# Kernel tuning notes

Hardware: AMD Instinct MI355X
Metric: run time of the kernel (lower is better)

## Reference

```python
import jax, jax.numpy as jnp
import numpy as np

B, DIN, DOUT, DC, K, DB = 4096, 512, 512, 64, 16, 256
NEG = 0.01
LN_EPS = 1e-5

def _lrelu(v):
    return jnp.where(v >= 0, v, NEG * v)

def setup_inputs() -> dict:
    key = jax.random.key(0)
    ks = jax.random.split(key, 12)
    bound = 1.0 / np.sqrt(DIN)
    def u(k, shape, b):
        return jax.random.uniform(k, shape, jnp.float32, -b, b)
    return {
        "x": jax.random.normal(ks[0], (B, DIN), jnp.float32),
        "c": jax.random.normal(ks[1], (B, DC), jnp.float32),
        "ln_gamma": jnp.ones((DIN,), jnp.float32),
        "ln_beta": jnp.zeros((DIN,), jnp.float32),
        "w1": u(ks[2], (DC, DB), 1.0 / np.sqrt(DC)),
        "b1": u(ks[3], (DB,), 1.0 / np.sqrt(DC)),
        "wr": u(ks[4], (DB, DB), 1.0 / np.sqrt(DB)),
        "br": u(ks[5], (DB,), 1.0 / np.sqrt(DB)),
        "w2": u(ks[6], (DB, K), 1.0 / np.sqrt(DB)),
        "b2": u(ks[7], (K,), 1.0 / np.sqrt(DB)),
        "W": u(ks[8], (K, DIN, DOUT), bound),
        "bvec": u(ks[9], (K, DOUT), bound),
    }

def reference(x, c, ln_gamma, ln_beta, w1, b1, wr, br, w2, b2, W, bvec):
    # DenseActivation: LayerNorm + LeakyReLU (dropout_rate=0)
    mu = jnp.mean(x, axis=-1, keepdims=True)
    var = jnp.mean(jnp.square(x - mu), axis=-1, keepdims=True)
    xn = (x - mu) * jax.lax.rsqrt(var + LN_EPS) * ln_gamma + ln_beta
    a = _lrelu(xn)  # [B, DIN]
    # basis_functions(c): Linear -> 1 preactivation resnet block -> LeakyReLU -> Linear
    h = c @ w1 + b1                      # [B, DB]
    h = h + (_lrelu(h) @ wr + br)        # residual block (preactivation)
    h = _lrelu(h)                        # activate_output
    bf = h @ w2 + b2                     # [B, K]
    # out_b = x_b^T (sum_k bf_bk W_k) + bf_b @ bias ; reordered contraction
    xw = jnp.einsum("bi,kio->bko", a, W)       # [B, K, DOUT]
    out = jnp.einsum("bk,bko->bo", bf, xw)     # [B, DOUT]
    out = out + bf @ bvec
    return out
```

## Files before the change

### kernel.cpp

```cpp
#include <hip/hip_runtime.h>


#define LRELU(v) ((v) >= 0.f ? (v) : 0.01f * (v))

typedef _Float16 f16x8 __attribute__((ext_vector_type(8)));
typedef float f32x4 __attribute__((ext_vector_type(4)));

#define GL16(gp, lp) __builtin_amdgcn_global_load_lds(                      \
    (const __attribute__((address_space(1))) void*)(gp),                    \
    (__attribute__((address_space(3))) void*)(lp), 16, 0, 0)

#define MFMA16(a, b, c) __builtin_amdgcn_mfma_f32_16x16x32_f16((a), (b), (c), 0, 0, 0)

__global__ __launch_bounds__(256) void prep_kernel(
    const float* __restrict__ x, const float* __restrict__ gam,
    const float* __restrict__ bet, _Float16* __restrict__ a,
    const float* __restrict__ c, const float* __restrict__ w1,
    const float* __restrict__ b1, const float* __restrict__ wr,
    const float* __restrict__ br, const float* __restrict__ w2,
    const float* __restrict__ b2, float* __restrict__ bfo,
    const float* __restrict__ W, _Float16* __restrict__ Wt)
{
    __shared__ __align__(16) char smem[18432];
    int tid = threadIdx.x;
    int blk = blockIdx.x;

    if (blk < 512) {
        float* c_l  = (float*)smem;
        float* lr_l = (float*)(smem + 2048);
        float* h_l  = (float*)(smem + 10240);
        int b0 = blk * 8;

        for (int i = tid; i < 8 * 64; i += 256) c_l[i] = c[(size_t)b0 * 64 + i];

        float w1c[64];
#pragma unroll
        for (int u = 0; u < 64; ++u) w1c[u] = w1[u * 256 + tid];
        float b1s = b1[tid];
        __syncthreads();

        float h1[8];
#pragma unroll
        for (int r = 0; r < 8; ++r) h1[r] = b1s;
#pragma unroll
        for (int j4 = 0; j4 < 16; ++j4) {
#pragma unroll
            for (int r = 0; r < 8; ++r) {
                float4 cv = *(const float4*)&c_l[r * 64 + j4 * 4];
                h1[r] += cv.x * w1c[j4 * 4 + 0] + cv.y * w1c[j4 * 4 + 1] +
                         cv.z * w1c[j4 * 4 + 2] + cv.w * w1c[j4 * 4 + 3];
            }
        }
#pragma unroll
        for (int r = 0; r < 8; ++r) lr_l[r * 256 + tid] = LRELU(h1[r]);
        __syncthreads();

        float brv = br[tid];
        float h2[8];
#pragma unroll
        for (int r = 0; r < 8; ++r) h2[r] = h1[r] + brv;

#pragma unroll 1
        for (int jc = 0; jc < 8; ++jc) {
            float w8[32];
#pragma unroll
            for (int u = 0; u < 32; ++u) w8[u] = wr[(jc * 32 + u) * 256 + tid];
#pragma unroll
            for (int j4 = 0; j4 < 8; ++j4) {
#pragma unroll
                for (int r = 0; r < 8; ++r) {
                    float4 lv = *(const float4*)&lr_l[r * 256 + jc * 32 + j4 * 4];
                    h2[r] += lv.x * w8[j4 * 4 + 0] + lv.y * w8[j4 * 4 + 1] +
                             lv.z * w8[j4 * 4 + 2] + lv.w * w8[j4 * 4 + 3];
                }
            }
        }
#pragma unroll
        for (int r = 0; r < 8; ++r) h_l[r * 256 + tid] = LRELU(h2[r]);
        __syncthreads();

        if (tid < 128) {
            int r = tid >> 4, k = tid & 15;
            float s = b2[k];
#pragma unroll 1
            for (int qc = 0; qc < 8; ++qc) {
                float wv[32];
#pragma unroll
                for (int u = 0; u < 32; ++u) wv[u] = w2[(qc * 32 + u) * 16 + k];
#pragma unroll
                for (int q4 = 0; q4 < 8; ++q4) {
                    float4 hv = *(const float4*)&h_l[r * 256 + qc * 32 + q4 * 4];
                    s += hv.x * wv[q4 * 4 + 0] + hv.y * wv[q4 * 4 + 1] +
                         hv.z * wv[q4 * 4 + 2] + hv.w * wv[q4 * 4 + 3];
                }
            }
            bfo[(size_t)(b0 + r) * 16 + k] = s;
        }

    } else if (blk < 1536) {
        float* t = (float*)smem;
        int bid = blk - 512;
        int k  = bid >> 6;
        int it = (bid >> 3) & 7;
        int ot = bid & 7;
        int i0 = it * 64, o0 = ot * 64;

        int rr = tid >> 4, c4 = (tid & 15) * 4;
#pragma unroll
        for (int p = 0; p < 4; ++p) {
            int r = p * 16 + rr;
            float4 v = *(const float4*)&W[((size_t)(k * 512 + i0 + r)) * 512 + o0 + c4];
            t[r * 65 + c4 + 0] = v.x;
            t[r * 65 + c4 + 1] = v.y;
            t[r * 65 + c4 + 2] = v.z;
            t[r * 65 + c4 + 3] = v.w;
        }
        __syncthreads();

        int ol = tid >> 2, c0 = (tid & 3) * 16;
        _Float16 hb[16] __attribute__((aligned(16)));
#pragma unroll
        for (int u = 0; u < 16; ++u) hb[u] = (_Float16)t[(c0 + u) * 65 + ol];
        _Float16* dst = &Wt[(size_t)(o0 + ol) * 8192 + k * 512 + i0 + c0];
        *(float4*)dst       = *(const float4*)&hb[0];
        *(float4*)(dst + 8) = *(const float4*)&hb[8];

    } else {
        int lane = tid & 63;
        int row  = (blk - 1536) * 4 + (tid >> 6);
        const float* xr = x + (size_t)row * 512 + lane * 8;
        float4 v0 = *(const float4*)xr;
        float4 v1 = *(const float4*)(xr + 4);

        float s = v0.x + v0.y + v0.z + v0.w + v1.x + v1.y + v1.z + v1.w;
#pragma unroll
        for (int m = 1; m < 64; m <<= 1) s += __shfl_xor(s, m);
        float mean = s * (1.f / 512.f);

        float d, s2 = 0.f;
        d = v0.x - mean; s2 += d * d;
        d = v0.y - mean; s2 += d * d;
        d = v0.z - mean; s2 += d * d;
        d = v0.w - mean; s2 += d * d;
        d = v1.x - mean; s2 += d * d;
        d = v1.y - mean; s2 += d * d;
        d = v1.z - mean; s2 += d * d;
        d = v1.w - mean; s2 += d * d;
#pragma unroll
        for (int m = 1; m < 64; m <<= 1) s2 += __shfl_xor(s2, m);
        float rstd = rsqrtf(s2 * (1.f / 512.f) + 1e-5f);

        float4 g0 = *(const float4*)&gam[lane * 8];
        float4 g1 = *(const float4*)&gam[lane * 8 + 4];
        float4 b0 = *(const float4*)&bet[lane * 8];
        float4 b1v = *(const float4*)&bet[lane * 8 + 4];

        _Float16 o8[8] __attribute__((aligned(16)));
        float y;
        y = (v0.x - mean) * rstd * g0.x + b0.x;  y = LRELU(y); o8[0] = (_Float16)y;
        y = (v0.y - mean) * rstd * g0.y + b0.y;  y = LRELU(y); o8[1] = (_Float16)y;
        y = (v0.z - mean) * rstd * g0.z + b0.z;  y = LRELU(y); o8[2] = (_Float16)y;
        y = (v0.w - mean) * rstd * g0.w + b0.w;  y = LRELU(y); o8[3] = (_Float16)y;
        y = (v1.x - mean) * rstd * g1.x + b1v.x; y = LRELU(y); o8[4] = (_Float16)y;
        y = (v1.y - mean) * rstd * g1.y + b1v.y; y = LRELU(y); o8[5] = (_Float16)y;
        y = (v1.z - mean) * rstd * g1.z + b1v.z; y = LRELU(y); o8[6] = (_Float16)y;
        y = (v1.w - mean) * rstd * g1.w + b1v.w; y = LRELU(y); o8[7] = (_Float16)y;

        *(float4*)&a[(size_t)row * 512 + lane * 8] = *(const float4*)o8;
    }
}

template <int NSPLIT>
__global__ __launch_bounds__(512, 2) void gemm_kernel(
    const _Float16* __restrict__ A,
    const _Float16* __restrict__ Wt,
    const float* __restrict__ bfg,
    const float* __restrict__ bvec,
    _Float16* __restrict__ pout)
{
    constexpr int KTN = 16 / NSPLIT;
    constexpr int NT  = KTN * 8;

    __shared__ _Float16 As[2][256 * 64];
    __shared__ _Float16 Bs[2][256 * 64];

    const int tid = threadIdx.x;
    const int bid = blockIdx.x;
    const int split = bid % NSPLIT;
    const int mn  = bid / NSPLIT;
    const int n0  = (mn & 1) * 256;
    const int bm0 = (mn >> 1) * 256;
    const int kt0 = split * KTN;

    const int lane = tid & 63, wid = tid >> 6;
    const int wm = wid >> 2, wn = wid & 3;
    const int l16 = lane & 15, lg = lane >> 4;

    _Float16 s16[KTN][8];
#pragma unroll
    for (int kt = 0; kt < KTN; ++kt)
#pragma unroll
        for (int f = 0; f < 8; ++f)
            s16[kt][f] = (_Float16)
                bfg[(size_t)(bm0 + wm * 128 + f * 16 + l16) * 16 + kt0 + kt];

    const int brow = tid >> 3;
    const int swc  = (tid & 7) ^ (brow & 7);
    const _Float16* aAs = A  + (size_t)(bm0 + brow) * 512  + swc * 8;
    const _Float16* aBs = Wt + (size_t)(n0  + brow) * 8192 + swc * 8;

    auto STAGE = [&](int t, int buf) {
        const int ka = (t & 7) * 64;
        const size_t kb = (size_t)(kt0 + (t >> 3)) * 512 + ka;
        char* la = (char*)&As[buf][0] + tid * 16;
        char* lb = (char*)&Bs[buf][0] + tid * 16;
#pragma unroll
        for (int p = 0; p < 4; ++p) {
            GL16(aAs + (size_t)(p * 64) * 512 + ka, la + p * 8192);
            GL16(aBs + (size_t)(p * 64) * 8192 + kb, lb + p * 8192);
        }
    };

    const int swr = l16 & 7;
    const int aRowByte = (wm * 128 + l16) * 128;
    const int bRowByte = (wn * 64 + l16) * 128;
    const int sw0 = ((0 + lg) ^ swr) << 4;
    const int sw1 = ((4 + lg) ^ swr) << 4;

    const f32x4 z4 = {0.f, 0.f, 0.f, 0.f};
    f32x4 acc[8][4];
#pragma unroll
    for (int f = 0; f < 8; ++f)
#pragma unroll
        for (int nf = 0; nf < 4; ++nf) acc[f][nf] = z4;

    STAGE(0, 0);
    STAGE(1, 1);
    asm volatile("s_waitcnt vmcnt(8)" ::: "memory");
    __builtin_amdgcn_s_barrier();
    __builtin_amdgcn_sched_barrier(0);

#define AREAD(q)                                                            \
    xa = *(const f16x8*)(Ab + aRowByte + (2 * (q) + 0) * 2048 + sw0);       \
    xb = *(const f16x8*)(Ab + aRowByte + (2 * (q) + 0) * 2048 + sw1);       \
    xc = *(const f16x8*)(Ab + aRowByte + (2 * (q) + 1) * 2048 + sw0);       \
    xd = *(const f16x8*)(Ab + aRowByte + (2 * (q) + 1) * 2048 + sw1);

#define MFMAQ(q)                                                            \
    {                                                                       \
        const _Float16 sA = s16[kt][2 * (q) + 0];                           \
        const _Float16 sB = s16[kt][2 * (q) + 1];                           \
        xa *= sA; xb *= sA; xc *= sB; xd *= sB;                             \
        __builtin_amdgcn_s_setprio(1);                                      \
        acc[2*(q)+0][0] = MFMA16(xa, bA0, acc[2*(q)+0][0]);                 \
        acc[2*(q)+0][0] = MFMA16(xb, bA1, acc[2*(q)+0][0]);                 \
        acc[2*(q)+0][1] = MFMA16(xa, bB0, acc[2*(q)+0][1]);                 \
        acc[2*(q)+0][1] = MFMA16(xb, bB1, acc[2*(q)+0][1]);                 \
        acc[2*(q)+0][2] = MFMA16(xa, bC0, acc[2*(q)+0][2]);                 \
        acc[2*(q)+0][2] = MFMA16(xb, bC1, acc[2*(q)+0][2]);                 \
        acc[2*(q)+0][3] = MFMA16(xa, bD0, acc[2*(q)+0][3]);                 \
        acc[2*(q)+0][3] = MFMA16(xb, bD1, acc[2*(q)+0][3]);                 \
        acc[2*(q)+1][0] = MFMA16(xc, bA0, acc[2*(q)+1][0]);                 \
        acc[2*(q)+1][0] = MFMA16(xd, bA1, acc[2*(q)+1][0]);                 \
        acc[2*(q)+1][1] = MFMA16(xc, bB0, acc[2*(q)+1][1]);                 \
        acc[2*(q)+1][1] = MFMA16(xd, bB1, acc[2*(q)+1][1]);                 \
        acc[2*(q)+1][2] = MFMA16(xc, bC0, acc[2*(q)+1][2]);                 \
        acc[2*(q)+1][2] = MFMA16(xd, bC1, acc[2*(q)+1][2]);                 \
        acc[2*(q)+1][3] = MFMA16(xc, bD0, acc[2*(q)+1][3]);                 \
        acc[2*(q)+1][3] = MFMA16(xd, bD1, acc[2*(q)+1][3]);                 \
        __builtin_amdgcn_s_setprio(0);                                      \
    }

#pragma unroll
    for (int kt = 0; kt < KTN; ++kt) {
#pragma unroll 1
        for (int t2 = 0; t2 < 8; ++t2) {
            const int t = kt * 8 + t2;
            const int cur = t & 1;
            const char* Ab = (const char*)&As[cur][0];
            const char* Bb = (const char*)&Bs[cur][0];
            const int tt = t + 2;
            const bool st = (tt < NT);
            char* sAd = (char*)&As[cur][0] + tid * 16;
            char* sBd = (char*)&Bs[cur][0] + tid * 16;
            const int ka = (tt & 7) * 64;
            const size_t kb = (size_t)(kt0 + (tt >> 3)) * 512 + ka;

            f16x8 xa, xb, xc, xd;

            f16x8 bA0 = *(const f16x8*)(Bb + bRowByte + 0 * 2048 + sw0);
            f16x8 bA1 = *(const f16x8*)(Bb + bRowByte + 0 * 2048 + sw1);
            f16x8 bB0 = *(const f16x8*)(Bb + bRowByte + 1 * 2048 + sw0);
            f16x8 bB1 = *(const f16x8*)(Bb + bRowByte + 1 * 2048 + sw1);
            f16x8 bC0 = *(const f16x8*)(Bb + bRowByte + 2 * 2048 + sw0);
            f16x8 bC1 = *(const f16x8*)(Bb + bRowByte + 2 * 2048 + sw1);
            f16x8 bD0 = *(const f16x8*)(Bb + bRowByte + 3 * 2048 + sw0);
            f16x8 bD1 = *(const f16x8*)(Bb + bRowByte + 3 * 2048 + sw1);
            AREAD(0);
            __builtin_amdgcn_s_barrier();
            MFMAQ(0);
            __builtin_amdgcn_s_barrier();

            AREAD(1);
            if (st) {
                GL16(aBs + (size_t)(0 * 64) * 8192 + kb, sBd + 0 * 8192);
                GL16(aBs + (size_t)(1 * 64) * 8192 + kb, sBd + 1 * 8192);
            }
            __builtin_amdgcn_s_barrier();
            MFMAQ(1);
            __builtin_amdgcn_s_barrier();

            AREAD(2);
            if (st) {
                GL16(aBs + (size_t)(2 * 64) * 8192 + kb, sBd + 2 * 8192);
                GL16(aBs + (size_t)(3 * 64) * 8192 + kb, sBd + 3 * 8192);
                GL16(aAs + (size_t)(0 * 64) * 512 + ka, sAd + 0 * 8192);
                GL16(aAs + (size_t)(2 * 64) * 512 + ka, sAd + 2 * 8192);
            }
            __builtin_amdgcn_s_barrier();
            MFMAQ(2);
            __builtin_amdgcn_s_barrier();

            AREAD(3);
            __builtin_amdgcn_s_barrier();
            MFMAQ(3);
            __builtin_amdgcn_s_barrier();

            if (st) {
                GL16(aAs + (size_t)(1 * 64) * 512 + ka, sAd + 1 * 8192);
                GL16(aAs + (size_t)(3 * 64) * 512 + ka, sAd + 3 * 8192);
                asm volatile("s_waitcnt vmcnt(8)" ::: "memory");
            } else {
                asm volatile("s_waitcnt vmcnt(0)" ::: "memory");
            }
            __builtin_amdgcn_s_barrier();
            __builtin_amdgcn_sched_barrier(0);
        }
    }
#undef AREAD
#undef MFMAQ

    _Float16* op = pout + (size_t)split * (4096 * 512);
    const int colBase = n0 + wn * 64 + l16;
    float bvv[KTN][4];
#pragma unroll
    for (int kt = 0; kt < KTN; ++kt)
#pragma unroll
        for (int nf = 0; nf < 4; ++nf)
            bvv[kt][nf] = bvec[(kt0 + kt) * 512 + colBase + nf * 16];

#pragma unroll
    for (int f = 0; f < 8; ++f)
#pragma unroll
        for (int j = 0; j < 4; ++j) {
            const int grow = bm0 + wm * 128 + f * 16 + lg * 4 + j;
            const float* bfr = &bfg[(size_t)grow * 16 + kt0];
            float bfl[KTN];
#pragma unroll
            for (int kt = 0; kt < KTN; ++kt) bfl[kt] = bfr[kt];
            _Float16* orow = op + (size_t)grow * 512 + colBase;
#pragma unroll
            for (int nf = 0; nf < 4; ++nf) {
                float v = acc[f][nf][j];
#pragma unroll
                for (int kt = 0; kt < KTN; ++kt) v += bfl[kt] * bvv[kt][nf];
                orow[nf * 16] = (_Float16)v;
            }
        }
}

__global__ __launch_bounds__(256) void reduce_kernel(const _Float16* __restrict__ p,
                                                     float* __restrict__ out,
                                                     int nsplit)
{
    size_t i   = (size_t)blockIdx.x * 256 + threadIdx.x;
    size_t off = i * 8;
    float s[8] = {0.f, 0.f, 0.f, 0.f, 0.f, 0.f, 0.f, 0.f};
    for (int sp = 0; sp < nsplit; ++sp) {
        f16x8 v = *(const f16x8*)&p[(size_t)sp * 2097152 + off];
#pragma unroll
        for (int u = 0; u < 8; ++u) s[u] += (float)v[u];
    }
    float4 o0 = {s[0], s[1], s[2], s[3]};
    float4 o1 = {s[4], s[5], s[6], s[7]};
    *(float4*)&out[off]     = o0;
    *(float4*)&out[off + 4] = o1;
}

extern "C" void kernel_launch(void* const* d_in, const int* in_sizes, int n_in,
                              void* d_out, int out_size, void* d_ws, size_t ws_size,
                              hipStream_t stream)
{
    const float* x    = (const float*)d_in[0];
    const float* c    = (const float*)d_in[1];
    const float* gam  = (const float*)d_in[2];
    const float* bet  = (const float*)d_in[3];
    const float* w1   = (const float*)d_in[4];
    const float* b1   = (const float*)d_in[5];
    const float* wr   = (const float*)d_in[6];
    const float* br   = (const float*)d_in[7];
    const float* w2   = (const float*)d_in[8];
    const float* b2   = (const float*)d_in[9];
    const float* W    = (const float*)d_in[10];
    const float* bvec = (const float*)d_in[11];
    float* out = (float*)d_out;

    const int nsplit = 8;
    const size_t partBytes = (size_t)nsplit * 4096 * 512 * sizeof(_Float16);

    char* ws = (char*)d_ws;
    _Float16* part = (_Float16*)ws;
    _Float16* Wt   = (_Float16*)(ws + partBytes);
    _Float16* af   = (_Float16*)(ws + partBytes + (8u << 20));
    float*    bf   = (float*)(ws + partBytes + (12u << 20));

    prep_kernel<<<dim3(2560), dim3(256), 0, stream>>>(
        x, gam, bet, af, c, w1, b1, wr, br, w2, b2, bf, W, Wt);

    gemm_kernel<8><<<dim3(256), dim3(512), 0, stream>>>(af, Wt, bf, bvec, part);

    reduce_kernel<<<dim3(1024), dim3(256), 0, stream>>>(part, out, nsplit);
}
```

Measured before the change: 84.40 us.

## Shrink GEMM tile to 128x128 with 256 threads and halve the K split

The fused GEMM moves from 256x256 tiles with 512 threads and an 8-way K split to 128x128 tiles with 256 threads and a 4-way split. The grid doubles to 512 blocks, each running twice as many K iterations, and the inner loop is restructured into two MFMA phases per stage instead of four. The smaller split means fewer partial fp16 outputs to write and reduce. The cost is lower data reuse per tile, which raises LDS and global traffic relative to MFMA work.

```diff
diff --git a/kernel.cpp b/kernel.cpp
--- a/kernel.cpp
+++ b/kernel.cpp
@@ -171,7 +171,7 @@
 }
 
 template <int NSPLIT>
-__global__ __launch_bounds__(512, 2) void gemm_kernel(
+__global__ __launch_bounds__(256, 2) void gemm_kernel(
     const _Float16* __restrict__ A,
     const _Float16* __restrict__ Wt,
     const float* __restrict__ bfg,
@@ -181,28 +181,28 @@
     constexpr int KTN = 16 / NSPLIT;
     constexpr int NT  = KTN * 8;
 
-    __shared__ _Float16 As[2][256 * 64];
-    __shared__ _Float16 Bs[2][256 * 64];
+    __shared__ _Float16 As[2][128 * 64];
+    __shared__ _Float16 Bs[2][128 * 64];
 
     const int tid = threadIdx.x;
     const int bid = blockIdx.x;
     const int split = bid % NSPLIT;
     const int mn  = bid / NSPLIT;
-    const int n0  = (mn & 1) * 256;
-    const int bm0 = (mn >> 1) * 256;
+    const int n0  = (mn & 3) * 128;
+    const int bm0 = (mn >> 2) * 128;
     const int kt0 = split * KTN;
 
     const int lane = tid & 63, wid = tid >> 6;
-    const int wm = wid >> 2, wn = wid & 3;
+    const int wm = wid >> 1, wn = wid & 1;
     const int l16 = lane & 15, lg = lane >> 4;
 
-    _Float16 s16[KTN][8];
+    _Float16 s16[KTN][4];
 #pragma unroll
     for (int kt = 0; kt < KTN; ++kt)
 #pragma unroll
-        for (int f = 0; f < 8; ++f)
+        for (int f = 0; f < 4; ++f)
             s16[kt][f] = (_Float16)
-                bfg[(size_t)(bm0 + wm * 128 + f * 16 + l16) * 16 + kt0 + kt];
+                bfg[(size_t)(bm0 + wm * 64 + f * 16 + l16) * 16 + kt0 + kt];
 
     const int brow = tid >> 3;
     const int swc  = (tid & 7) ^ (brow & 7);
@@ -216,21 +216,21 @@
         char* lb = (char*)&Bs[buf][0] + tid * 16;
 #pragma unroll
         for (int p = 0; p < 4; ++p) {
-            GL16(aAs + (size_t)(p * 64) * 512 + ka, la + p * 8192);
-            GL16(aBs + (size_t)(p * 64) * 8192 + kb, lb + p * 8192);
+            GL16(aAs + (size_t)(p * 32) * 512 + ka, la + p * 4096);
+            GL16(aBs + (size_t)(p * 32) * 8192 + kb, lb + p * 4096);
         }
     };
 
     const int swr = l16 & 7;
-    const int aRowByte = (wm * 128 + l16) * 128;
+    const int aRowByte = (wm * 64 + l16) * 128;
     const int bRowByte = (wn * 64 + l16) * 128;
     const int sw0 = ((0 + lg) ^ swr) << 4;
     const int sw1 = ((4 + lg) ^ swr) << 4;
 
     const f32x4 z4 = {0.f, 0.f, 0.f, 0.f};
-    f32x4 acc[8][4];
-#pragma unroll
-    for (int f = 0; f < 8; ++f)
+    f32x4 acc[4][4];
+#pragma unroll
+    for (int f = 0; f < 4; ++f)
 #pragma unroll
         for (int nf = 0; nf < 4; ++nf) acc[f][nf] = z4;
 
@@ -239,37 +239,6 @@
     asm volatile("s_waitcnt vmcnt(8)" ::: "memory");
     __builtin_amdgcn_s_barrier();
     __builtin_amdgcn_sched_barrier(0);
-
-#define AREAD(q)                                                            \
-    xa = *(const f16x8*)(Ab + aRowByte + (2 * (q) + 0) * 2048 + sw0);       \
-    xb = *(const f16x8*)(Ab + aRowByte + (2 * (q) + 0) * 2048 + sw1);       \
-    xc = *(const f16x8*)(Ab + aRowByte + (2 * (q) + 1) * 2048 + sw0);       \
-    xd = *(const f16x8*)(Ab + aRowByte + (2 * (q) + 1) * 2048 + sw1);
-
-#define MFMAQ(q)                                                            \
-    {                                                                       \
-        const _Float16 sA = s16[kt][2 * (q) + 0];                           \
-        const _Float16 sB = s16[kt][2 * (q) + 1];                           \
-        xa *= sA; xb *= sA; xc *= sB; xd *= sB;                             \
-        __builtin_amdgcn_s_setprio(1);                                      \
-        acc[2*(q)+0][0] = MFMA16(xa, bA0, acc[2*(q)+0][0]);                 \
-        acc[2*(q)+0][0] = MFMA16(xb, bA1, acc[2*(q)+0][0]);                 \
-        acc[2*(q)+0][1] = MFMA16(xa, bB0, acc[2*(q)+0][1]);                 \
-        acc[2*(q)+0][1] = MFMA16(xb, bB1, acc[2*(q)+0][1]);                 \
-        acc[2*(q)+0][2] = MFMA16(xa, bC0, acc[2*(q)+0][2]);                 \
-        acc[2*(q)+0][2] = MFMA16(xb, bC1, acc[2*(q)+0][2]);                 \
-        acc[2*(q)+0][3] = MFMA16(xa, bD0, acc[2*(q)+0][3]);                 \
-        acc[2*(q)+0][3] = MFMA16(xb, bD1, acc[2*(q)+0][3]);                 \
-        acc[2*(q)+1][0] = MFMA16(xc, bA0, acc[2*(q)+1][0]);                 \
-        acc[2*(q)+1][0] = MFMA16(xd, bA1, acc[2*(q)+1][0]);                 \
-        acc[2*(q)+1][1] = MFMA16(xc, bB0, acc[2*(q)+1][1]);                 \
-        acc[2*(q)+1][1] = MFMA16(xd, bB1, acc[2*(q)+1][1]);                 \
-        acc[2*(q)+1][2] = MFMA16(xc, bC0, acc[2*(q)+1][2]);                 \
-        acc[2*(q)+1][2] = MFMA16(xd, bC1, acc[2*(q)+1][2]);                 \
-        acc[2*(q)+1][3] = MFMA16(xc, bD0, acc[2*(q)+1][3]);                 \
-        acc[2*(q)+1][3] = MFMA16(xd, bD1, acc[2*(q)+1][3]);                 \
-        __builtin_amdgcn_s_setprio(0);                                      \
-    }
 
 #pragma unroll
     for (int kt = 0; kt < KTN; ++kt) {
@@ -286,8 +255,6 @@
             const int ka = (tt & 7) * 64;
             const size_t kb = (size_t)(kt0 + (tt >> 3)) * 512 + ka;
 
-            f16x8 xa, xb, xc, xd;
-
             f16x8 bA0 = *(const f16x8*)(Bb + bRowByte + 0 * 2048 + sw0);
             f16x8 bA1 = *(const f16x8*)(Bb + bRowByte + 0 * 2048 + sw1);
             f16x8 bB0 = *(const f16x8*)(Bb + bRowByte + 1 * 2048 + sw0);
@@ -296,39 +263,77 @@
             f16x8 bC1 = *(const f16x8*)(Bb + bRowByte + 2 * 2048 + sw1);
             f16x8 bD0 = *(const f16x8*)(Bb + bRowByte + 3 * 2048 + sw0);
             f16x8 bD1 = *(const f16x8*)(Bb + bRowByte + 3 * 2048 + sw1);
-            AREAD(0);
+            f16x8 a00 = *(const f16x8*)(Ab + aRowByte + 0 * 2048 + sw0);
+            f16x8 a01 = *(const f16x8*)(Ab + aRowByte + 0 * 2048 + sw1);
+            f16x8 a10 = *(const f16x8*)(Ab + aRowByte + 1 * 2048 + sw0);
+            f16x8 a11 = *(const f16x8*)(Ab + aRowByte + 1 * 2048 + sw1);
             __builtin_amdgcn_s_barrier();
-            MFMAQ(0);
+
+            {
+                const _Float16 s0 = s16[kt][0], s1 = s16[kt][1];
+                a00 *= s0; a01 *= s0; a10 *= s1; a11 *= s1;
+                __builtin_amdgcn_s_setprio(1);
+                acc[0][0] = MFMA16(a00, bA0, acc[0][0]);
+                acc[0][0] = MFMA16(a01, bA1, acc[0][0]);
+                acc[0][1] = MFMA16(a00, bB0, acc[0][1]);
+                acc[0][1] = MFMA16(a01, bB1, acc[0][1]);
+                acc[0][2] = MFMA16(a00, bC0, acc[0][2]);
+                acc[0][2] = MFMA16(a01, bC1, acc[0][2]);
+                acc[0][3] = MFMA16(a00, bD0, acc[0][3]);
+                acc[0][3] = MFMA16(a01, bD1, acc[0][3]);
+                acc[1][0] = MFMA16(a10, bA0, acc[1][0]);
+                acc[1][0] = MFMA16(a11, bA1, acc[1][0]);
+                acc[1][1] = MFMA16(a10, bB0, acc[1][1]);
+                acc[1][1] = MFMA16(a11, bB1, acc[1][1]);
+                acc[1][2] = MFMA16(a10, bC0, acc[1][2]);
+                acc[1][2] = MFMA16(a11, bC1, acc[1][2]);
+                acc[1][3] = MFMA16(a10, bD0, acc[1][3]);
+                acc[1][3] = MFMA16(a11, bD1, acc[1][3]);
+                __builtin_amdgcn_s_setprio(0);
+            }
             __builtin_amdgcn_s_barrier();
 
-            AREAD(1);
+            f16x8 a20 = *(const f16x8*)(Ab + aRowByte + 2 * 2048 + sw0);
+            f16x8 a21 = *(const f16x8*)(Ab + aRowByte + 2 * 2048 + sw1);
+            f16x8 a30 = *(const f16x8*)(Ab + aRowByte + 3 * 2048 + sw0);
+            f16x8 a31 = *(const f16x8*)(Ab + aRowByte + 3 * 2048 + sw1);
             if (st) {
-                GL16(aBs + (size_t)(0 * 64) * 8192 + kb, sBd + 0 * 8192);
-                GL16(aBs + (size_t)(1 * 64) * 8192 + kb, sBd + 1 * 8192);
+                GL16(aBs + (size_t)(0 * 32) * 8192 + kb, sBd + 0 * 4096);
+                GL16(aBs + (size_t)(1 * 32) * 8192 + kb, sBd + 1 * 4096);
+                GL16(aBs + (size_t)(2 * 32) * 8192 + kb, sBd + 2 * 4096);
+                GL16(aBs + (size_t)(3 * 32) * 8192 + kb, sBd + 3 * 4096);
+                GL16(aAs + (size_t)(0 * 32) * 512 + ka, sAd + 0 * 4096);
+                GL16(aAs + (size_t)(2 * 32) * 512 + ka, sAd + 2 * 4096);
             }
             __builtin_amdgcn_s_barrier();
-            MFMAQ(1);
+
+            {
+                const _Float16 s2 = s16[kt][2], s3 = s16[kt][3];
+                a20 *= s2; a21 *= s2; a30 *= s3; a31 *= s3;
+                __builtin_amdgcn_s_setprio(1);
+                acc[2][0] = MFMA16(a20, bA0, acc[2][0]);
+                acc[2][0] = MFMA16(a21, bA1, acc[2][0]);
+                acc[2][1] = MFMA16(a20, bB0, acc[2][1]);
+                acc[2][1] = MFMA16(a21, bB1, acc[2][1]);
+                acc[2][2] = MFMA16(a20, bC0, acc[2][2]);
+                acc[2][2] = MFMA16(a21, bC1, acc[2][2]);
+                acc[2][3] = MFMA16(a20, bD0, acc[2][3]);
+                acc[2][3] = MFMA16(a21, bD1, acc[2][3]);
+                acc[3][0] = MFMA16(a30, bA0, acc[3][0]);
+                acc[3][0] = MFMA16(a31, bA1, acc[3][0]);
+                acc[3][1] = MFMA16(a30, bB0, acc[3][1]);
+                acc[3][1] = MFMA16(a31, bB1, acc[3][1]);
+                acc[3][2] = MFMA16(a30, bC0, acc[3][2]);
+                acc[3][2] = MFMA16(a31, bC1, acc[3][2]);
+                acc[3][3] = MFMA16(a30, bD0, acc[3][3]);
+                acc[3][3] = MFMA16(a31, bD1, acc[3][3]);
+                __builtin_amdgcn_s_setprio(0);
+            }
             __builtin_amdgcn_s_barrier();
 
-            AREAD(2);
             if (st) {
-                GL16(aBs + (size_t)(2 * 64) * 8192 + kb, sBd + 2 * 8192);
-                GL16(aBs + (size_t)(3 * 64) * 8192 + kb, sBd + 3 * 8192);
-                GL16(aAs + (size_t)(0 * 64) * 512 + ka, sAd + 0 * 8192);
-                GL16(aAs + (size_t)(2 * 64) * 512 + ka, sAd + 2 * 8192);
-            }
-            __builtin_amdgcn_s_barrier();
-            MFMAQ(2);
-            __builtin_amdgcn_s_barrier();
-
-            AREAD(3);
-            __builtin_amdgcn_s_barrier();
-            MFMAQ(3);
-            __builtin_amdgcn_s_barrier();
-
-            if (st) {
-                GL16(aAs + (size_t)(1 * 64) * 512 + ka, sAd + 1 * 8192);
-                GL16(aAs + (size_t)(3 * 64) * 512 + ka, sAd + 3 * 8192);
+                GL16(aAs + (size_t)(1 * 32) * 512 + ka, sAd + 1 * 4096);
+                GL16(aAs + (size_t)(3 * 32) * 512 + ka, sAd + 3 * 4096);
                 asm volatile("s_waitcnt vmcnt(8)" ::: "memory");
             } else {
                 asm volatile("s_waitcnt vmcnt(0)" ::: "memory");
@@ -337,8 +342,6 @@
             __builtin_amdgcn_sched_barrier(0);
         }
     }
-#undef AREAD
-#undef MFMAQ
 
     _Float16* op = pout + (size_t)split * (4096 * 512);
     const int colBase = n0 + wn * 64 + l16;
@@ -350,10 +353,10 @@
             bvv[kt][nf] = bvec[(kt0 + kt) * 512 + colBase + nf * 16];
 
 #pragma unroll
-    for (int f = 0; f < 8; ++f)
+    for (int f = 0; f < 4; ++f)
 #pragma unroll
         for (int j = 0; j < 4; ++j) {
-            const int grow = bm0 + wm * 128 + f * 16 + lg * 4 + j;
+            const int grow = bm0 + wm * 64 + f * 16 + lg * 4 + j;
             const float* bfr = &bfg[(size_t)grow * 16 + kt0];
             float bfl[KTN];
 #pragma unroll
@@ -405,7 +408,7 @@
     const float* bvec = (const float*)d_in[11];
     float* out = (float*)d_out;
 
-    const int nsplit = 8;
+    const int nsplit = 4;
     const size_t partBytes = (size_t)nsplit * 4096 * 512 * sizeof(_Float16);
 
     char* ws = (char*)d_ws;
@@ -417,7 +420,7 @@
     prep_kernel<<<dim3(2560), dim3(256), 0, stream>>>(
         x, gam, bet, af, c, w1, b1, wr, br, w2, b2, bf, W, Wt);
 
-    gemm_kernel<8><<<dim3(256), dim3(512), 0, stream>>>(af, Wt, bf, bvec, part);
+    gemm_kernel<4><<<dim3(512), dim3(256), 0, stream>>>(af, Wt, bf, bvec, part);
 
     reduce_kernel<<<dim3(1024), dim3(256), 0, stream>>>(part, out, nsplit);
 }
```

Result: no change. 82.89 us (median of 2 runs) (-1.8%).
